# Kernel tuning notes

Measured on AMD Instinct MI355X. Metric: run time of the kernel, lower is better.

Reference implementation:

```python
import jax, jax.numpy as jnp
import numpy as np

B, DIM, F, H = 16384, 64, 8, 8
D2 = DIM // 2


def setup_inputs() -> dict:
    key = jax.random.key(0)
    ks = jax.random.split(key, 8)
    s = 0.1  # small init so exp(s_net) stays well-conditioned
    return {
        "x": jax.random.normal(ks[0], (B, DIM), jnp.float32),
        "x_star": jax.random.normal(ks[1], (B, DIM), jnp.float32),
        "W0": jax.random.normal(ks[2], (F, 4, H, D2), jnp.float32) * s,
        "b0": jax.random.normal(ks[3], (F, 4, H), jnp.float32) * s,
        "W1": jax.random.normal(ks[4], (F, 4, H, H), jnp.float32) * s,
        "b1": jax.random.normal(ks[5], (F, 4, H), jnp.float32) * s,
        "W2": jax.random.normal(ks[6], (F, 4, D2, H), jnp.float32) * s,
        "b2": jax.random.normal(ks[7], (F, 4, D2), jnp.float32) * s,
    }


def _fcnn(v, w0, c0, w1, c1, w2, c2):
    # FCNN: Linear -> Tanh -> Linear -> Tanh -> Linear, on a single vector v [D2]
    h = jnp.tanh(w0 @ v + c0)
    h = jnp.tanh(w1 @ h + c1)
    return w2 @ h + c2


def _phi(v, params):
    # Chain of n_flows RealNVP coupling layers on a single sample v [DIM].
    def step(v, p):
        W0, b0, W1, b1, W2, b2 = p  # leading axis 4 = (t1, s1, t2, s2)
        lo, up = v[:D2], v[D2:]
        t1 = _fcnn(lo, W0[0], b0[0], W1[0], b1[0], W2[0], b2[0])
        s1 = _fcnn(lo, W0[1], b0[1], W1[1], b1[1], W2[1], b2[1])
        up = t1 + up * jnp.exp(s1)
        t2 = _fcnn(up, W0[2], b0[2], W1[2], b1[2], W2[2], b2[2])
        s2 = _fcnn(up, W0[3], b0[3], W1[3], b1[3], W2[3], b2[3])
        lo = t2 + lo * jnp.exp(s2)
        return jnp.concatenate([lo, up]), None

    z, _ = jax.lax.scan(step, v, params)
    return z


def reference(x, x_star, W0, b0, W1, b1, W2, b2):
    params = (W0, b0, W1, b1, W2, b2)
    # Per-sample Jacobian of the flow (replaces torch autograd loop): [B, DIM, DIM]
    jac = jax.vmap(jax.jacfwd(lambda v: _phi(v, params)))(x)
    # -grad of quadratic potential (feature=None): -2 * (x - x_star)
    g = -2.0 * (x - x_star)
    # torch.solve(potential_grad, phi_jac): solve J u = g per sample
    return jnp.linalg.solve(jac, g[..., None])[..., 0]
```

## Files before the change

### kernel.cpp

```cpp
#include <hip/hip_runtime.h>


namespace {

typedef __fp16 f16x2 __attribute__((ext_vector_type(2)));
typedef __fp16 v4h __attribute__((ext_vector_type(4)));
typedef __fp16 v8h __attribute__((ext_vector_type(8)));
typedef float f32x4 __attribute__((ext_vector_type(4)));
typedef unsigned int u32;
typedef u32 u32x2 __attribute__((ext_vector_type(2)));
typedef u32 u32x4 __attribute__((ext_vector_type(4)));

constexpr int NB = 16384;

__device__ __forceinline__ float frcp(float x) { return __builtin_amdgcn_rcpf(x); }
__device__ __forceinline__ float ftanh(float x) {
  float e = __expf(2.f * x);
  return 1.f - 2.f * frcp(e + 1.f);
}
__device__ __forceinline__ f16x2 pk(float a, float b) {
  return __builtin_amdgcn_cvt_pkrtz(a, b);
}
__device__ __forceinline__ v8h mk8(f16x2 a, f16x2 b, f16x2 c, f16x2 d) {
  const u32x4 t = {__builtin_bit_cast(u32, a), __builtin_bit_cast(u32, b),
                   __builtin_bit_cast(u32, c), __builtin_bit_cast(u32, d)};
  return __builtin_bit_cast(v8h, t);
}
__device__ __forceinline__ v4h mk4(f16x2 a, f16x2 b) {
  const u32x2 t = {__builtin_bit_cast(u32, a), __builtin_bit_cast(u32, b)};
  return __builtin_bit_cast(v4h, t);
}

__device__ __forceinline__ int pbase(int p) {
  return ((p >> 1) << 2) + ((p & 1) << 1);
}

}

#define L3_FWD(P, BB, D0, D1, D2, D3)                                         \
  do {                                                                        \
    const bool act_ = ((BB) < 2) == (q < 2);                                  \
    v4h Ab = *(const v4h*)(LW2 + ((P)*256 + (BB)*64 + abbase));               \
    Ab = act_ ? Ab : z4;                                                      \
    const f32x4 cb = *(const f32x4*)(LB2 + ((P)*4 + (BB)) * 16 + q * 4);      \
    const f32x4 ob =                                                          \
        __builtin_amdgcn_mfma_f32_16x16x16f16(Ab, H2v, cb, 0, 0, 0);          \
    D0 = ob[0]; D1 = ob[1]; D2 = ob[2]; D3 = ob[3];                           \
  } while (0)

#define FWD_UPD(J, W) W##J = fmaf(W##J, __expf(s##J), t##J)

#define FWD_HALF(P, V, W)                                                     \
  do {                                                                        \
    const v8h Bq = mk8(pk(V##0, V##1), pk(V##2, V##3), pk(V##4, V##5),        \
                       pk(V##6, V##7));                                       \
    const v8h A0 = *(const v8h*)(LW0 + (((P)*64 + q * 16 + n) << 2));         \
    const f32x4 c0 = *(const f32x4*)(LB0 + (P)*16 + q * 4);                   \
    f32x4 d1 = __builtin_amdgcn_mfma_f32_16x16x32_f16(A0, Bq, c0, 0, 0, 0);   \
    const f16x2 H1a = pk(ftanh(d1[0]), ftanh(d1[1]));                         \
    const f16x2 H1b = pk(ftanh(d1[2]), ftanh(d1[3]));                         \
    v4h A1 = *(const v4h*)(LW1 + ((P)*64 + a1off));                           \
    A1 = act1 ? A1 : z4;                                                      \
    const f32x4 c1 = *(const f32x4*)(LB1 + (P)*16 + q * 4);                   \
    f32x4 d2 =                                                                \
        __builtin_amdgcn_mfma_f32_16x16x16f16(A1, mk4(H1a, H1b), c1, 0, 0, 0);\
    const f16x2 H2a = pk(ftanh(d2[0]), ftanh(d2[1]));                         \
    const f16x2 H2b = pk(ftanh(d2[2]), ftanh(d2[3]));                         \
    const v4h H2v = mk4(H2a, H2b);                                            \
    if (n < 8) {                                                              \
      const float4 pkd = {__builtin_bit_cast(float, H1a),                     \
                          __builtin_bit_cast(float, H1b),                     \
                          __builtin_bit_cast(float, H2a),                     \
                          __builtin_bit_cast(float, H2b)};                    \
      sHC[(P)*128 + hcb] = pkd;                                               \
    }                                                                         \
    float t0, t1, t2, t3, t4, t5, t6, t7;                                     \
    float s0, s1, s2, s3, s4, s5, s6, s7;                                     \
    L3_FWD(P, 0, t0, t1, t2, t3);                                             \
    L3_FWD(P, 1, t4, t5, t6, t7);                                             \
    L3_FWD(P, 2, s0, s1, s2, s3);                                             \
    L3_FWD(P, 3, s4, s5, s6, s7);                                             \
    FWD_UPD(0, W); FWD_UPD(1, W); FWD_UPD(2, W); FWD_UPD(3, W);               \
    FWD_UPD(4, W); FWD_UPD(5, W); FWD_UPD(6, W); FWD_UPD(7, W);               \
  } while (0)

#define L3_BWD(P, BB, D0, D1, D2, D3, J0, J1, J2, J3)                         \
  do {                                                                        \
    const bool act_ = ((BB) < 2) == (q < 2);                                  \
    v4h Ab = *(const v4h*)(LW2 + ((P)*256 + (BB)*64 + abbase));               \
    Ab = act_ ? Ab : z4;                                                      \
    const f32x4 cb = *(const f32x4*)(LB2 + ((P)*4 + (BB)) * 16 + q * 4);      \
    const f32x4 ob =                                                          \
        __builtin_amdgcn_mfma_f32_16x16x16f16(Ab, H2v, cb, 0, 0, 0);          \
    const f32x4 jb =                                                          \
        __builtin_amdgcn_mfma_f32_16x16x16f16(Ab, G2v, zc, 0, 0, 0);          \
    D0 = ob[0]; D1 = ob[1]; D2 = ob[2]; D3 = ob[3];                           \
    J0 = jb[0]; J1 = jb[1]; J2 = jb[2]; J3 = jb[3];                           \
  } while (0)

#define BWD_INV(J, ST, DME)                                                   \
  do {                                                                        \
    const float esi_ = __expf(-s##J);                                         \
    const float dd_ = ST##J - t##J;                                           \
    ST##J = dd_ * esi_;                                                       \
    DME##J = (DME##J - ut##J - dd_ * us##J) * esi_;                           \
  } while (0)

#define BWD_HALF(P, ST, DME, DOT)                                             \
  do {                                                                        \
    const float4 pkd = sHC[(P)*128 + hcb];                                    \
    const f16x2 H1a = __builtin_bit_cast(f16x2, pkd.x);                       \
    const f16x2 H1b = __builtin_bit_cast(f16x2, pkd.y);                       \
    const f16x2 H2a = __builtin_bit_cast(f16x2, pkd.z);                       \
    const f16x2 H2b = __builtin_bit_cast(f16x2, pkd.w);                       \
    const v8h Bu = mk8(pk(DOT##0, DOT##1), pk(DOT##2, DOT##3),                \
                       pk(DOT##4, DOT##5), pk(DOT##6, DOT##7));               \
    const v8h A0 = *(const v8h*)(LW0 + (((P)*64 + q * 16 + n) << 2));         \
    f32x4 d1u = __builtin_amdgcn_mfma_f32_16x16x32_f16(A0, Bu, zc, 0, 0, 0);  \
    const float h10 = (float)H1a[0], h11 = (float)H1a[1];                     \
    const float h12 = (float)H1b[0], h13 = (float)H1b[1];                     \
    const f16x2 G1a =                                                         \
        pk((1.f - h10 * h10) * d1u[0], (1.f - h11 * h11) * d1u[1]);           \
    const f16x2 G1b =                                                         \
        pk((1.f - h12 * h12) * d1u[2], (1.f - h13 * h13) * d1u[3]);           \
    v4h A1 = *(const v4h*)(LW1 + ((P)*64 + a1off));                           \
    A1 = act1 ? A1 : z4;                                                      \
    f32x4 d2u =                                                               \
        __builtin_amdgcn_mfma_f32_16x16x16f16(A1, mk4(G1a, G1b), zc, 0, 0, 0);\
    const float h20 = (float)H2a[0], h21 = (float)H2a[1];                     \
    const float h22 = (float)H2b[0], h23 = (float)H2b[1];                     \
    const f16x2 G2a =                                                         \
        pk((1.f - h20 * h20) * d2u[0], (1.f - h21 * h21) * d2u[1]);           \
    const f16x2 G2b =                                                         \
        pk((1.f - h22 * h22) * d2u[2], (1.f - h23 * h23) * d2u[3]);           \
    const v4h H2v = mk4(H2a, H2b);                                            \
    const v4h G2v = mk4(G2a, G2b);                                            \
    float t0, t1, t2, t3, t4, t5, t6, t7;                                     \
    float s0, s1, s2, s3, s4, s5, s6, s7;                                     \
    float ut0, ut1, ut2, ut3, ut4, ut5, ut6, ut7;                             \
    float us0, us1, us2, us3, us4, us5, us6, us7;                             \
    L3_BWD(P, 0, t0, t1, t2, t3, ut0, ut1, ut2, ut3);                         \
    L3_BWD(P, 1, t4, t5, t6, t7, ut4, ut5, ut6, ut7);                         \
    L3_BWD(P, 2, s0, s1, s2, s3, us0, us1, us2, us3);                         \
    L3_BWD(P, 3, s4, s5, s6, s7, us4, us5, us6, us7);                         \
    BWD_INV(0, ST, DME); BWD_INV(1, ST, DME);                                 \
    BWD_INV(2, ST, DME); BWD_INV(3, ST, DME);                                 \
    BWD_INV(4, ST, DME); BWD_INV(5, ST, DME);                                 \
    BWD_INV(6, ST, DME); BWD_INV(7, ST, DME);                                 \
  } while (0)

__global__ __attribute__((amdgpu_flat_work_group_size(256, 256),
                          amdgpu_waves_per_eu(2, 2))) void nf_policy_kernel(
    const float* __restrict__ x, const float* __restrict__ xs,
    const float* __restrict__ gW0, const float* __restrict__ gb0,
    const float* __restrict__ gW1, const float* __restrict__ gb1,
    const float* __restrict__ gW2, const float* __restrict__ gb2,
    float* __restrict__ out) {
  __shared__ __align__(16) f16x2 LW0[4096];
  __shared__ __align__(16) f16x2 LW1[1024];
  __shared__ __align__(16) f16x2 LW2[4096];
  __shared__ __align__(16) float LB0[256];
  __shared__ __align__(16) float LB1[256];
  __shared__ __align__(16) float LB2[1024];
  __shared__ __align__(16) float4 sHC[2048];

  const int tid = threadIdx.x;
  for (int i = tid; i < 4096; i += 256) {
    const int p = i >> 8, rem = i & 255, qq = rem >> 6, rem2 = rem & 63;
    const int mm = rem2 >> 2, w = rem2 & 3;
    const int net = pbase(p) + (mm >> 3);
    const int h = mm & 7, k0 = qq * 8 + w * 2;
    const float* src = gW0 + net * 256 + h * 32 + k0;
    LW0[i] = pk(src[0], src[1]);
  }
  for (int i = tid; i < 1024; i += 256) {
    const int p = i >> 6, rem = i & 63, half = rem >> 5;
    const int row = (rem >> 2) & 7, kk = rem & 3;
    const int net = pbase(p) + half;
    const float* src = gW1 + net * 64 + row * 8 + kk * 2;
    LW1[i] = pk(src[0], src[1]);
  }
  for (int i = tid; i < 4096; i += 256) {
    const int p = i >> 8, rem = i & 255, b = rem >> 6, rem2 = rem & 63;
    const int mm = rem2 >> 2, kk = rem2 & 3;
    const int net = pbase(p) + (b >> 1);
    const int d = 8 * (mm >> 2) + ((b & 1) << 2) + (mm & 3);
    const float* src = gW2 + net * 256 + d * 8 + kk * 2;
    LW2[i] = pk(src[0], src[1]);
  }
  for (int i = tid; i < 256; i += 256) {
    const int p = i >> 4, mm = i & 15;
    const int net = pbase(p) + (mm >> 3);
    LB0[i] = gb0[net * 8 + (mm & 7)];
    LB1[i] = gb1[net * 8 + (mm & 7)];
  }
  for (int i = tid; i < 1024; i += 256) {
    const int p = i >> 6, b = (i >> 4) & 3, mm = i & 15;
    const int net = pbase(p) + (b >> 1);
    const int d = 8 * (mm >> 2) + ((b & 1) << 2) + (mm & 3);
    LB2[i] = gb2[net * 32 + d];
  }
  __syncthreads();

  const int lane = tid & 63;
  const int wv = tid >> 6;
  const int n = lane & 15;
  const int q = lane >> 4;
  const int e = blockIdx.x * 32 + wv * 8 + (n & 7);
  const int hcb = wv * 32 + q * 8 + (n & 7);

  const v4h z4 = {(__fp16)0.f, (__fp16)0.f, (__fp16)0.f, (__fp16)0.f};
  const f32x4 zc = {0.f, 0.f, 0.f, 0.f};
  const bool act1 = (n < 8) == (q < 2);
  const int a1off = ((n & 7) << 2) + ((q & 1) << 1) + ((n >= 8) ? 32 : 0);
  const int abbase = n * 4 + ((q & 1) << 1);

  float lo0, lo1, lo2, lo3, lo4, lo5, lo6, lo7;
  float up0, up1, up2, up3, up4, up5, up6, up7;
  float av0, av1, av2, av3, av4, av5, av6, av7;
  float bv0, bv1, bv2, bv3, bv4, bv5, bv6, bv7;
  {
    const float* xe = x + (size_t)e * 64;
    const float* se = xs + (size_t)e * 64;
    const float4 a0 = *(const float4*)(xe + q * 8);
    const float4 a1 = *(const float4*)(xe + q * 8 + 4);
    const float4 u0 = *(const float4*)(xe + 32 + q * 8);
    const float4 u1 = *(const float4*)(xe + 32 + q * 8 + 4);
    const float4 p0 = *(const float4*)(se + q * 8);
    const float4 p1 = *(const float4*)(se + q * 8 + 4);
    const float4 r0 = *(const float4*)(se + 32 + q * 8);
    const float4 r1 = *(const float4*)(se + 32 + q * 8 + 4);
    lo0 = a0.x; lo1 = a0.y; lo2 = a0.z; lo3 = a0.w;
    lo4 = a1.x; lo5 = a1.y; lo6 = a1.z; lo7 = a1.w;
    up0 = u0.x; up1 = u0.y; up2 = u0.z; up3 = u0.w;
    up4 = u1.x; up5 = u1.y; up6 = u1.z; up7 = u1.w;
    av0 = -2.f * (a0.x - p0.x); av1 = -2.f * (a0.y - p0.y);
    av2 = -2.f * (a0.z - p0.z); av3 = -2.f * (a0.w - p0.w);
    av4 = -2.f * (a1.x - p1.x); av5 = -2.f * (a1.y - p1.y);
    av6 = -2.f * (a1.z - p1.z); av7 = -2.f * (a1.w - p1.w);
    bv0 = -2.f * (u0.x - r0.x); bv1 = -2.f * (u0.y - r0.y);
    bv2 = -2.f * (u0.z - r0.z); bv3 = -2.f * (u0.w - r0.w);
    bv4 = -2.f * (u1.x - r1.x); bv5 = -2.f * (u1.y - r1.y);
    bv6 = -2.f * (u1.z - r1.z); bv7 = -2.f * (u1.w - r1.w);
  }

#pragma clang loop unroll(disable)
  for (int st = 0; st < 8; ++st) {
    const int p0i = 2 * st;
    FWD_HALF(p0i, lo, up);
    FWD_HALF(p0i + 1, up, lo);
  }

#pragma clang loop unroll(disable)
  for (int st = 7; st >= 0; --st) {
    const int p0i = 2 * st;
    BWD_HALF(p0i + 1, lo, av, bv);
    BWD_HALF(p0i, up, bv, av);
  }

  if (n < 8) {
    float* oe = out + (size_t)e * 64;
    float4 v;
    v.x = av0; v.y = av1; v.z = av2; v.w = av3;
    *(float4*)(oe + q * 8) = v;
    v.x = av4; v.y = av5; v.z = av6; v.w = av7;
    *(float4*)(oe + q * 8 + 4) = v;
    v.x = bv0; v.y = bv1; v.z = bv2; v.w = bv3;
    *(float4*)(oe + 32 + q * 8) = v;
    v.x = bv4; v.y = bv5; v.z = bv6; v.w = bv7;
    *(float4*)(oe + 32 + q * 8 + 4) = v;
  }
}

extern "C" void kernel_launch(void* const* d_in, const int* in_sizes, int n_in,
                              void* d_out, int out_size, void* d_ws,
                              size_t ws_size, hipStream_t stream) {
  const float* x  = (const float*)d_in[0];
  const float* xs = (const float*)d_in[1];
  const float* W0 = (const float*)d_in[2];
  const float* b0 = (const float*)d_in[3];
  const float* W1 = (const float*)d_in[4];
  const float* b1 = (const float*)d_in[5];
  const float* W2 = (const float*)d_in[6];
  const float* b2 = (const float*)d_in[7];
  float* out = (float*)d_out;

  dim3 grid(NB / 32);
  dim3 block(256);
  nf_policy_kernel<<<grid, block, 0, stream>>>(x, xs, W0, b0, W1, b1, W2, b2,
                                               out);
}
```

Before: 98.92 us.

## Recompute hidden activations in backward pass instead of caching in LDS, double block size

The backward pass now recomputes the layer-1 and layer-2 tanh activations from the restored coupling inputs rather than reading them from a large shared-memory cache. This removes the LDS stores and loads and the 32 KB buffer. The block grows to 512 threads with each wave covering 4 samples instead of 8, and the waves-per-EU bounds are raised to allow more resident waves. The cost is an extra MFMA and tanh per layer in the backward pass, plus more duplicated lanes per useful sample, in exchange for better latency hiding.

```diff
diff --git a/kernel.cpp b/kernel.cpp
--- a/kernel.cpp
+++ b/kernel.cpp
@@ -67,13 +67,6 @@
     const f16x2 H2a = pk(ftanh(d2[0]), ftanh(d2[1]));                         \
     const f16x2 H2b = pk(ftanh(d2[2]), ftanh(d2[3]));                         \
     const v4h H2v = mk4(H2a, H2b);                                            \
-    if (n < 8) {                                                              \
-      const float4 pkd = {__builtin_bit_cast(float, H1a),                     \
-                          __builtin_bit_cast(float, H1b),                     \
-                          __builtin_bit_cast(float, H2a),                     \
-                          __builtin_bit_cast(float, H2b)};                    \
-      sHC[(P)*128 + hcb] = pkd;                                               \
-    }                                                                         \
     float t0, t1, t2, t3, t4, t5, t6, t7;                                     \
     float s0, s1, s2, s3, s4, s5, s6, s7;                                     \
     L3_FWD(P, 0, t0, t1, t2, t3);                                             \
@@ -106,34 +99,38 @@
     DME##J = (DME##J - ut##J - dd_ * us##J) * esi_;                           \
   } while (0)
 
-#define BWD_HALF(P, ST, DME, DOT)                                             \
-  do {                                                                        \
-    const float4 pkd = sHC[(P)*128 + hcb];                                    \
-    const f16x2 H1a = __builtin_bit_cast(f16x2, pkd.x);                       \
-    const f16x2 H1b = __builtin_bit_cast(f16x2, pkd.y);                       \
-    const f16x2 H2a = __builtin_bit_cast(f16x2, pkd.z);                       \
-    const f16x2 H2b = __builtin_bit_cast(f16x2, pkd.w);                       \
+#define BWD_HALF(P, ST, DME, DOT, VIN)                                        \
+  do {                                                                        \
+    const v8h Bv = mk8(pk(VIN##0, VIN##1), pk(VIN##2, VIN##3),                \
+                       pk(VIN##4, VIN##5), pk(VIN##6, VIN##7));               \
     const v8h Bu = mk8(pk(DOT##0, DOT##1), pk(DOT##2, DOT##3),                \
                        pk(DOT##4, DOT##5), pk(DOT##6, DOT##7));               \
     const v8h A0 = *(const v8h*)(LW0 + (((P)*64 + q * 16 + n) << 2));         \
+    const f32x4 c0 = *(const f32x4*)(LB0 + (P)*16 + q * 4);                   \
+    f32x4 d1 = __builtin_amdgcn_mfma_f32_16x16x32_f16(A0, Bv, c0, 0, 0, 0);   \
     f32x4 d1u = __builtin_amdgcn_mfma_f32_16x16x32_f16(A0, Bu, zc, 0, 0, 0);  \
-    const float h10 = (float)H1a[0], h11 = (float)H1a[1];                     \
-    const float h12 = (float)H1b[0], h13 = (float)H1b[1];                     \
+    const float h10 = ftanh(d1[0]), h11 = ftanh(d1[1]);                       \
+    const float h12 = ftanh(d1[2]), h13 = ftanh(d1[3]);                       \
+    const f16x2 H1a = pk(h10, h11);                                           \
+    const f16x2 H1b = pk(h12, h13);                                           \
     const f16x2 G1a =                                                         \
         pk((1.f - h10 * h10) * d1u[0], (1.f - h11 * h11) * d1u[1]);           \
     const f16x2 G1b =                                                         \
         pk((1.f - h12 * h12) * d1u[2], (1.f - h13 * h13) * d1u[3]);           \
     v4h A1 = *(const v4h*)(LW1 + ((P)*64 + a1off));                           \
     A1 = act1 ? A1 : z4;                                                      \
+    const f32x4 c1 = *(const f32x4*)(LB1 + (P)*16 + q * 4);                   \
+    f32x4 d2 =                                                                \
+        __builtin_amdgcn_mfma_f32_16x16x16f16(A1, mk4(H1a, H1b), c1, 0, 0, 0);\
     f32x4 d2u =                                                               \
         __builtin_amdgcn_mfma_f32_16x16x16f16(A1, mk4(G1a, G1b), zc, 0, 0, 0);\
-    const float h20 = (float)H2a[0], h21 = (float)H2a[1];                     \
-    const float h22 = (float)H2b[0], h23 = (float)H2b[1];                     \
+    const float h20 = ftanh(d2[0]), h21 = ftanh(d2[1]);                       \
+    const float h22 = ftanh(d2[2]), h23 = ftanh(d2[3]);                       \
     const f16x2 G2a =                                                         \
         pk((1.f - h20 * h20) * d2u[0], (1.f - h21 * h21) * d2u[1]);           \
     const f16x2 G2b =                                                         \
         pk((1.f - h22 * h22) * d2u[2], (1.f - h23 * h23) * d2u[3]);           \
-    const v4h H2v = mk4(H2a, H2b);                                            \
+    const v4h H2v = mk4(pk(h20, h21), pk(h22, h23));                          \
     const v4h G2v = mk4(G2a, G2b);                                            \
     float t0, t1, t2, t3, t4, t5, t6, t7;                                     \
     float s0, s1, s2, s3, s4, s5, s6, s7;                                     \
@@ -149,8 +146,8 @@
     BWD_INV(6, ST, DME); BWD_INV(7, ST, DME);                                 \
   } while (0)
 
-__global__ __attribute__((amdgpu_flat_work_group_size(256, 256),
-                          amdgpu_waves_per_eu(2, 2))) void nf_policy_kernel(
+__global__ __attribute__((amdgpu_flat_work_group_size(512, 512),
+                          amdgpu_waves_per_eu(4, 8))) void nf_policy_kernel(
     const float* __restrict__ x, const float* __restrict__ xs,
     const float* __restrict__ gW0, const float* __restrict__ gb0,
     const float* __restrict__ gW1, const float* __restrict__ gb1,
@@ -162,10 +159,9 @@
   __shared__ __align__(16) float LB0[256];
   __shared__ __align__(16) float LB1[256];
   __shared__ __align__(16) float LB2[1024];
-  __shared__ __align__(16) float4 sHC[2048];
 
   const int tid = threadIdx.x;
-  for (int i = tid; i < 4096; i += 256) {
+  for (int i = tid; i < 4096; i += 512) {
     const int p = i >> 8, rem = i & 255, qq = rem >> 6, rem2 = rem & 63;
     const int mm = rem2 >> 2, w = rem2 & 3;
     const int net = pbase(p) + (mm >> 3);
@@ -173,14 +169,14 @@
     const float* src = gW0 + net * 256 + h * 32 + k0;
     LW0[i] = pk(src[0], src[1]);
   }
-  for (int i = tid; i < 1024; i += 256) {
+  for (int i = tid; i < 1024; i += 512) {
     const int p = i >> 6, rem = i & 63, half = rem >> 5;
     const int row = (rem >> 2) & 7, kk = rem & 3;
     const int net = pbase(p) + half;
     const float* src = gW1 + net * 64 + row * 8 + kk * 2;
     LW1[i] = pk(src[0], src[1]);
   }
-  for (int i = tid; i < 4096; i += 256) {
+  for (int i = tid; i < 4096; i += 512) {
     const int p = i >> 8, rem = i & 255, b = rem >> 6, rem2 = rem & 63;
     const int mm = rem2 >> 2, kk = rem2 & 3;
     const int net = pbase(p) + (b >> 1);
@@ -188,13 +184,13 @@
     const float* src = gW2 + net * 256 + d * 8 + kk * 2;
     LW2[i] = pk(src[0], src[1]);
   }
-  for (int i = tid; i < 256; i += 256) {
+  for (int i = tid; i < 256; i += 512) {
     const int p = i >> 4, mm = i & 15;
     const int net = pbase(p) + (mm >> 3);
     LB0[i] = gb0[net * 8 + (mm & 7)];
     LB1[i] = gb1[net * 8 + (mm & 7)];
   }
-  for (int i = tid; i < 1024; i += 256) {
+  for (int i = tid; i < 1024; i += 512) {
     const int p = i >> 6, b = (i >> 4) & 3, mm = i & 15;
     const int net = pbase(p) + (b >> 1);
     const int d = 8 * (mm >> 2) + ((b & 1) << 2) + (mm & 3);
@@ -206,8 +202,7 @@
   const int wv = tid >> 6;
   const int n = lane & 15;
   const int q = lane >> 4;
-  const int e = blockIdx.x * 32 + wv * 8 + (n & 7);
-  const int hcb = wv * 32 + q * 8 + (n & 7);
+  const int e = blockIdx.x * 32 + wv * 4 + (n & 3);
 
   const v4h z4 = {(__fp16)0.f, (__fp16)0.f, (__fp16)0.f, (__fp16)0.f};
   const f32x4 zc = {0.f, 0.f, 0.f, 0.f};
@@ -254,11 +249,11 @@
 #pragma clang loop unroll(disable)
   for (int st = 7; st >= 0; --st) {
     const int p0i = 2 * st;
-    BWD_HALF(p0i + 1, lo, av, bv);
-    BWD_HALF(p0i, up, bv, av);
-  }
-
-  if (n < 8) {
+    BWD_HALF(p0i + 1, lo, av, bv, up);
+    BWD_HALF(p0i, up, bv, av, lo);
+  }
+
+  if (n < 4) {
     float* oe = out + (size_t)e * 64;
     float4 v;
     v.x = av0; v.y = av1; v.z = av2; v.w = av3;
@@ -286,7 +281,7 @@
   float* out = (float*)d_out;
 
   dim3 grid(NB / 32);
-  dim3 block(256);
+  dim3 block(512);
   nf_policy_kernel<<<grid, block, 0, stream>>>(x, xs, W0, b0, W1, b1, W2, b2,
                                                out);
 }
```

After: 108.8 us. +10.0%, slower.
